# Kernel optimization log

Hardware: AMD Instinct MI355X
Metric: run time of the kernel (lower is better)

## Reference

```python
import jax, jax.numpy as jnp
import numpy as np


def setup_inputs() -> dict:
    key = jax.random.key(0)
    ks = jax.random.split(key, 5)
    B, DEC, ENC, H = 4, 256, 256, 512  # feature_dim = hl_size = 512, mlp hidden = 512
    decoder_states = jax.random.normal(ks[0], (B, DEC, H), dtype=jnp.float32)
    encoder_states = jax.random.normal(ks[1], (B, ENC, H), dtype=jnp.float32)
    ext_mask = jnp.zeros((B, DEC, ENC), dtype=bool)  # self.mask set externally; all-False here
    W_mlp = jax.random.normal(ks[2], (2 * H, H), dtype=jnp.float32) * 0.02  # Linear(2H -> H)
    b_mlp = jnp.zeros((H,), dtype=jnp.float32)
    W_out = jax.random.normal(ks[3], (H, 1), dtype=jnp.float32) * 0.02  # Linear(H -> 1)
    b_out = jnp.zeros((1,), dtype=jnp.float32)
    return {"decoder_states": decoder_states, "encoder_states": encoder_states,
            "ext_mask": ext_mask, "W_mlp": W_mlp, "b_mlp": b_mlp,
            "W_out": W_out, "b_out": b_out}


def reference(decoder_states, encoder_states, ext_mask, W_mlp, b_mlp, W_out, b_out):
    # decoder_states: [B, dec, H]; encoder_states: [B, enc, H]
    H = encoder_states.shape[-1]
    # pad mask: positions where encoder feature-0 equals 0.0 -> [B, 1, enc]
    pad_mask = (encoder_states == 0.0)[:, :, :1]
    pad_mask = jnp.swapaxes(pad_mask, 1, 2)  # [B, 1, enc]
    # cat(enc, dec) @ W_mlp  ==  enc @ W_mlp[:H] + dec @ W_mlp[H:]  (avoids 2H concat)
    enc_proj = jnp.einsum('beh,hm->bem', encoder_states, W_mlp[:H])   # [B, enc, Hm]
    dec_proj = jnp.einsum('bdh,hm->bdm', decoder_states, W_mlp[H:])   # [B, dec, Hm]
    hidden = jnp.tanh(dec_proj[:, :, None, :] + enc_proj[:, None, :, :] + b_mlp)  # [B, dec, enc, Hm]
    attn = jnp.einsum('bdem,mo->bde', hidden, W_out) + b_out[0]       # [B, dec, enc]
    attn = jnp.where(ext_mask, -jnp.inf, attn)
    attn = jnp.where(pad_mask, -jnp.inf, attn)
    attn = jax.nn.softmax(attn, axis=-1)
    context = jnp.einsum('bde,beh->bdh', attn, encoder_states)        # [B, dec, H]
    return (context, attn)
```

## Files before the change

kernel.cpp:

```cpp
#include <hip/hip_runtime.h>
#include <math.h>

#define B 4
#define DEC 256
#define ENC 256
#define HDIM 512

#define TANH_SCALE 2.8853900817779268f
#define LOG2E 1.4426950408889634f

__device__ __forceinline__ float fast_exp2(float x) { return __builtin_amdgcn_exp2f(x); }
__device__ __forceinline__ float fast_rcp(float x)  { return __builtin_amdgcn_rcpf(x); }

typedef __attribute__((ext_vector_type(8))) short bf16x8;
typedef __attribute__((ext_vector_type(4))) short bf16x4;
typedef __attribute__((ext_vector_type(4))) float f32x4;

__device__ __forceinline__ unsigned short bf16_rne(float x) {
    unsigned u = __float_as_uint(x);
    return (unsigned short)((u + 0x7FFFu + ((u >> 16) & 1u)) >> 16);
}
__device__ __forceinline__ float bf16_to_f(unsigned short h) {
    return __uint_as_float((unsigned)h << 16);
}

#define W_OFS(m, k) ((((long)(m) >> 4) << 13) + (((long)(k) >> 3) << 7) + (((m) & 15) << 3) + ((k) & 7))

__global__ __launch_bounds__(256) void convert_kernel(
    const float* __restrict__ enc, const float* __restrict__ dec,
    const float* __restrict__ Wmlp,
    unsigned short* __restrict__ Xh_e, unsigned short* __restrict__ Xl_e,
    unsigned short* __restrict__ Xh_d, unsigned short* __restrict__ Xl_d,
    unsigned short* __restrict__ Wh_e, unsigned short* __restrict__ Wl_e,
    unsigned short* __restrict__ Wh_d, unsigned short* __restrict__ Wl_d)
{
    const int tid = threadIdx.x, z = blockIdx.z;
    if (z < 2) {
        const float* X = z ? dec : enc;
        unsigned short* H = z ? Xh_d : Xh_e;
        unsigned short* L = z ? Xl_d : Xl_e;
        const long i8 = ((long)blockIdx.x * 256 + tid) * 8;
        float4 v0 = *(const float4*)(X + i8);
        float4 v1 = *(const float4*)(X + i8 + 4);
        float xs[8] = {v0.x, v0.y, v0.z, v0.w, v1.x, v1.y, v1.z, v1.w};
        bf16x8 hv, lv;
#pragma unroll
        for (int j = 0; j < 8; ++j) {
            unsigned short h = bf16_rne(xs[j]);
            hv[j] = (short)h;
            lv[j] = (short)bf16_rne(xs[j] - bf16_to_f(h));
        }
        *(bf16x8*)(H + i8) = hv;
        *(bf16x8*)(L + i8) = lv;
    } else {
        const float* Wsrc = Wmlp + (z == 3 ? (long)HDIM * HDIM : 0);
        unsigned short* H = (z == 3) ? Wh_d : Wh_e;
        unsigned short* L = (z == 3) ? Wl_d : Wl_e;
        const int t = blockIdx.x * 256 + tid;
        const int m = t & 511;
        const int k0 = (t >> 9) << 2;
        bf16x4 hv, lv;
#pragma unroll
        for (int j = 0; j < 4; ++j) {
            float x = Wsrc[(long)(k0 + j) * 512 + m];
            unsigned short h = bf16_rne(x);
            hv[j] = (short)h;
            lv[j] = (short)bf16_rne(x - bf16_to_f(h));
        }
        const long ofs = W_OFS(m, k0);
        *(bf16x4*)(H + ofs) = hv;
        *(bf16x4*)(L + ofs) = lv;
    }
}

__global__ __launch_bounds__(256) void proj_mfma_kernel(
    const unsigned short* __restrict__ Xh_e, const unsigned short* __restrict__ Xl_e,
    const unsigned short* __restrict__ Xh_d, const unsigned short* __restrict__ Xl_d,
    const unsigned short* __restrict__ Wh_e, const unsigned short* __restrict__ Wl_e,
    const unsigned short* __restrict__ Wh_d, const unsigned short* __restrict__ Wl_d,
    const float* __restrict__ bmlp,
    float* __restrict__ ET, float* __restrict__ Dmat)
{
    const int tid = threadIdx.x;
    const int wave = tid >> 6, lane = tid & 63;
    const int z = blockIdx.z;
    const int r0w = blockIdx.x * 64 + wave * 16;
    const int m0 = blockIdx.y * 32;
    const unsigned short* Xh = z ? Xh_d : Xh_e;
    const unsigned short* Xl = z ? Xl_d : Xl_e;
    const unsigned short* Wh = z ? Wh_d : Wh_e;
    const unsigned short* Wl = z ? Wl_d : Wl_e;

    const int col = lane & 15;
    const int quad = lane >> 4;

    const unsigned short* pah = Xh + (long)(r0w + col) * 512 + quad * 8;
    const unsigned short* pal = Xl + (long)(r0w + col) * 512 + quad * 8;
    const long bofs = ((long)(m0 >> 4) << 13) + (quad << 7) + (col << 3);
    const unsigned short* pb0h = Wh + bofs;
    const unsigned short* pb0l = Wl + bofs;
    const unsigned short* pb1h = Wh + bofs + 8192;
    const unsigned short* pb1l = Wl + bofs + 8192;

    f32x4 a0h = {0.f,0.f,0.f,0.f}, a0x = {0.f,0.f,0.f,0.f};
    f32x4 a1h = {0.f,0.f,0.f,0.f}, a1x = {0.f,0.f,0.f,0.f};

    bf16x8 Ah = *(const bf16x8*)pah,  Al = *(const bf16x8*)pal;
    bf16x8 B0h = *(const bf16x8*)pb0h, B0l = *(const bf16x8*)pb0l;
    bf16x8 B1h = *(const bf16x8*)pb1h, B1l = *(const bf16x8*)pb1l;

#pragma unroll 1
    for (int k0 = 0; k0 < 512; k0 += 32) {
        bf16x8 nAh = Ah, nAl = Al, nB0h = B0h, nB0l = B0l, nB1h = B1h, nB1l = B1l;
        if (k0 + 32 < 512) {
            nAh = *(const bf16x8*)(pah + k0 + 32);
            nAl = *(const bf16x8*)(pal + k0 + 32);
            const long ko = (long)(k0 + 32) << 4;
            nB0h = *(const bf16x8*)(pb0h + ko);
            nB0l = *(const bf16x8*)(pb0l + ko);
            nB1h = *(const bf16x8*)(pb1h + ko);
            nB1l = *(const bf16x8*)(pb1l + ko);
        }
        a0h = __builtin_amdgcn_mfma_f32_16x16x32_bf16(Ah, B0h, a0h, 0, 0, 0);
        a1h = __builtin_amdgcn_mfma_f32_16x16x32_bf16(Ah, B1h, a1h, 0, 0, 0);
        a0x = __builtin_amdgcn_mfma_f32_16x16x32_bf16(Ah, B0l, a0x, 0, 0, 0);
        a1x = __builtin_amdgcn_mfma_f32_16x16x32_bf16(Ah, B1l, a1x, 0, 0, 0);
        a0x = __builtin_amdgcn_mfma_f32_16x16x32_bf16(Al, B0h, a0x, 0, 0, 0);
        a1x = __builtin_amdgcn_mfma_f32_16x16x32_bf16(Al, B1h, a1x, 0, 0, 0);
        Ah = nAh; Al = nAl; B0h = nB0h; B0l = nB0l; B1h = nB1h; B1l = nB1l;
    }

    if (z == 0) {
        const int batch = r0w >> 8;
        const int e0 = (r0w & 255) + quad * 4;
        float* base = ET + (long)batch * HDIM * ENC;
        float4 v;
        v.x = fast_exp2((a0h[0] + a0x[0]) * TANH_SCALE);
        v.y = fast_exp2((a0h[1] + a0x[1]) * TANH_SCALE);
        v.z = fast_exp2((a0h[2] + a0x[2]) * TANH_SCALE);
        v.w = fast_exp2((a0h[3] + a0x[3]) * TANH_SCALE);
        *(float4*)&base[(long)(m0 + col) * ENC + e0] = v;
        v.x = fast_exp2((a1h[0] + a1x[0]) * TANH_SCALE);
        v.y = fast_exp2((a1h[1] + a1x[1]) * TANH_SCALE);
        v.z = fast_exp2((a1h[2] + a1x[2]) * TANH_SCALE);
        v.w = fast_exp2((a1h[3] + a1x[3]) * TANH_SCALE);
        *(float4*)&base[(long)(m0 + 16 + col) * ENC + e0] = v;
    } else {
        const float bq0 = bmlp[m0 + col];
        const float bq1 = bmlp[m0 + 16 + col];
        const int r = r0w + quad * 4;
#pragma unroll
        for (int i = 0; i < 4; ++i) {
            Dmat[(long)(r + i) * HDIM + m0 + col] =
                fast_exp2((a0h[i] + a0x[i] + bq0) * TANH_SCALE);
            Dmat[(long)(r + i) * HDIM + m0 + 16 + col] =
                fast_exp2((a1h[i] + a1x[i] + bq1) * TANH_SCALE);
        }
    }
}

__global__ __launch_bounds__(256) void attn_partial_kernel(
    const float* __restrict__ Dmat, const float* __restrict__ ET,
    const float* __restrict__ wo, float* __restrict__ part)
{
    __shared__ __align__(16) float ds[4][128];
    __shared__ __align__(16) float wos[128];

    const int tid = threadIdx.x;
    const int b = blockIdx.z, d0 = blockIdx.x * 4, mq = blockIdx.y;
    const int m0q = mq * 128;

    const float* Drow = Dmat + ((long)b * DEC + d0) * HDIM + m0q;
    if (tid < 128) {
#pragma unroll
        for (int r = 0; r < 4; ++r)
            ds[r][tid] = Drow[(long)r * HDIM + tid];
        wos[tid] = wo[m0q + tid];
    }

    const float* ecol = ET + (long)b * HDIM * ENC + (long)m0q * ENC + tid;

    float ev[16], nv[16];
#pragma unroll
    for (int j = 0; j < 16; ++j) ev[j] = ecol[j * ENC];
    __syncthreads();

    float acc[4] = {0.f, 0.f, 0.f, 0.f};
    for (int m = 0; m < 128; m += 16) {
        if (m + 16 < 128) {
#pragma unroll
            for (int j = 0; j < 16; ++j) nv[j] = ecol[(m + 16 + j) * ENC];
        }
        float4 dv[4][4], wv[4];
#pragma unroll
        for (int q = 0; q < 4; ++q) {
#pragma unroll
            for (int r = 0; r < 4; ++r)
                dv[r][q] = *(const float4*)&ds[r][m + q * 4];
            wv[q] = *(const float4*)&wos[m + q * 4];
        }
#pragma unroll
        for (int j = 0; j < 16; ++j) {
            float w = ((const float*)&wv[j >> 2])[j & 3];
#pragma unroll
            for (int r = 0; r < 4; ++r) {
                float t = fmaf(ev[j], ((const float*)&dv[r][j >> 2])[j & 3], 1.0f);
                acc[r] = fmaf(w, fast_rcp(t), acc[r]);
            }
        }
#pragma unroll
        for (int j = 0; j < 16; ++j) ev[j] = nv[j];
    }

    float* pq = part + (long)mq * (B * DEC * ENC);
#pragma unroll
    for (int r = 0; r < 4; ++r)
        pq[((long)b * DEC + d0 + r) * ENC + tid] = acc[r];
}

__global__ __launch_bounds__(256) void attn_finish_kernel(
    const float* __restrict__ part,
    const float* __restrict__ enc, const unsigned char* __restrict__ extm,
    float* __restrict__ attn_out)
{
    __shared__ float red[2][4][2];
    const int tid = threadIdx.x, lane = tid & 63, wave = tid >> 6;
    const int b = blockIdx.y, d0 = blockIdx.x * 2;
    const long g0 = (long)b * DEC + d0;
    const long NQ = (long)B * DEC * ENC;

    float a0 = 0.f, a1 = 0.f;
#pragma unroll
    for (int q = 0; q < 4; ++q) {
        a0 += part[q * NQ + g0 * ENC + tid];
        a1 += part[q * NQ + (g0 + 1) * ENC + tid];
    }

    const int e = tid;
    const bool pad = (enc[((long)b * ENC + e) * HDIM] == 0.0f);
    const bool x0m = extm[g0 * ENC + e] != 0;
    const bool x1m = extm[(g0 + 1) * ENC + e] != 0;
    float l0 = (pad || x0m) ? -__builtin_inff() : -2.0f * a0;
    float l1 = (pad || x1m) ? -__builtin_inff() : -2.0f * a1;

    float m0 = l0, m1 = l1;
#pragma unroll
    for (int off = 32; off >= 1; off >>= 1) {
        m0 = fmaxf(m0, __shfl_xor(m0, off, 64));
        m1 = fmaxf(m1, __shfl_xor(m1, off, 64));
    }
    if (lane == 0) { red[0][wave][0] = m0; red[0][wave][1] = m1; }
    __syncthreads();
    const float gm0 = fmaxf(fmaxf(red[0][0][0], red[0][1][0]), fmaxf(red[0][2][0], red[0][3][0]));
    const float gm1 = fmaxf(fmaxf(red[0][0][1], red[0][1][1]), fmaxf(red[0][2][1], red[0][3][1]));
    float p0 = fast_exp2((l0 - gm0) * LOG2E);
    float p1 = fast_exp2((l1 - gm1) * LOG2E);
    float s0 = p0, s1 = p1;
#pragma unroll
    for (int off = 32; off >= 1; off >>= 1) {
        s0 += __shfl_xor(s0, off, 64);
        s1 += __shfl_xor(s1, off, 64);
    }
    if (lane == 0) { red[1][wave][0] = s0; red[1][wave][1] = s1; }
    __syncthreads();
    const float gs0 = red[1][0][0] + red[1][1][0] + red[1][2][0] + red[1][3][0];
    const float gs1 = red[1][0][1] + red[1][1][1] + red[1][2][1] + red[1][3][1];
    attn_out[g0 * ENC + e] = p0 * fast_rcp(gs0);
    attn_out[(g0 + 1) * ENC + e] = p1 * fast_rcp(gs1);
}

#define C5_LOADW(WB, KOFF)                                                  \
    _Pragma("unroll")                                                       \
    for (int kk = 0; kk < 8; ++kk)                                          \
        WB[kk] = *(const float4*)&We[(long)((KOFF) + kk) * HDIM];

#define C5_FMA(WB, KOFF)                                                    \
    _Pragma("unroll")                                                       \
    for (int q = 0; q < 2; ++q) {                                           \
        float4 xq0 = *(const float4*)&as8[r0l][(KOFF) + q * 4];             \
        float4 xq1 = *(const float4*)&as8[r0l + 1][(KOFF) + q * 4];         \
        _Pragma("unroll")                                                   \
        for (int kk = 0; kk < 4; ++kk) {                                    \
            float4 w = WB[q * 4 + kk];                                      \
            float xv0 = ((const float*)&xq0)[kk];                           \
            float xv1 = ((const float*)&xq1)[kk];                           \
            acc[0][0] = fmaf(xv0, w.x, acc[0][0]);                          \
            acc[0][1] = fmaf(xv0, w.y, acc[0][1]);                          \
            acc[0][2] = fmaf(xv0, w.z, acc[0][2]);                          \
            acc[0][3] = fmaf(xv0, w.w, acc[0][3]);                          \
            acc[1][0] = fmaf(xv1, w.x, acc[1][0]);                          \
            acc[1][1] = fmaf(xv1, w.y, acc[1][1]);                          \
            acc[1][2] = fmaf(xv1, w.z, acc[1][2]);                          \
            acc[1][3] = fmaf(xv1, w.w, acc[1][3]);                          \
        }                                                                   \
    }

__global__ __launch_bounds__(256) void context_kernel(
    const float* __restrict__ attn, const float* __restrict__ enc,
    float* __restrict__ ctx)
{
    __shared__ __align__(16) float as8[8][ENC];
    const int tid = threadIdx.x;
    const int tx = tid & 63, ty = tid >> 6;
    const int r0 = blockIdx.x * 8;
    const int b = r0 >> 8;
    const int h0 = blockIdx.y * 256 + tx * 4;
    const int r0l = ty * 2;
    const float* We = enc + (long)b * ENC * HDIM + h0;

    {
        const float* ag = attn + (long)r0 * ENC;
#pragma unroll
        for (int i = 0; i < 2; ++i) {
            int idx = (tid + i * 256) * 4;
            *(float4*)&as8[0][idx] = *(const float4*)&ag[idx];
        }
    }

    float acc[2][4] = {};
    float4 Wa[8], Wb[8];
    C5_LOADW(Wa, 0)
    __syncthreads();

    for (int k0 = 0; k0 < ENC; k0 += 16) {
        C5_LOADW(Wb, k0 + 8)
        C5_FMA(Wa, k0)
        if (k0 + 16 < ENC) { C5_LOADW(Wa, k0 + 16) }
        C5_FMA(Wb, k0 + 8)
    }

#pragma unroll
    for (int i = 0; i < 2; ++i)
        *(float4*)&ctx[(long)(r0 + r0l + i) * HDIM + h0] =
            make_float4(acc[i][0], acc[i][1], acc[i][2], acc[i][3]);
}

extern "C" void kernel_launch(void* const* d_in, const int* in_sizes, int n_in,
                              void* d_out, int out_size, void* d_ws, size_t ws_size,
                              hipStream_t stream) {
    const float* dec = (const float*)d_in[0];
    const float* enc = (const float*)d_in[1];
    const unsigned char* extm = (const unsigned char*)d_in[2];
    const float* Wmlp = (const float*)d_in[3];
    const float* bmlp = (const float*)d_in[4];
    const float* Wout = (const float*)d_in[5];

    float* ctx = (float*)d_out;
    float* attn = ctx + (size_t)B * DEC * HDIM;

    const size_t F = (size_t)B * DEC * HDIM;
    float* ET = (float*)d_ws;
    float* Dmat = ET + F;
    unsigned short* Xh_e = (unsigned short*)(Dmat + F);
    unsigned short* Xl_e = Xh_e + F;
    unsigned short* Xh_d = Xl_e + F;
    unsigned short* Xl_d = Xh_d + F;
    unsigned short* Wh_e = Xl_d + F;
    unsigned short* Wl_e = Wh_e + HDIM * HDIM;
    unsigned short* Wh_d = Wl_e + HDIM * HDIM;
    unsigned short* Wl_d = Wh_d + HDIM * HDIM;
    float* part = (float*)(Wl_d + HDIM * HDIM);

    convert_kernel<<<dim3(256, 1, 4), 256, 0, stream>>>(
        enc, dec, Wmlp, Xh_e, Xl_e, Xh_d, Xl_d, Wh_e, Wl_e, Wh_d, Wl_d);
    proj_mfma_kernel<<<dim3(16, 16, 2), 256, 0, stream>>>(
        Xh_e, Xl_e, Xh_d, Xl_d, Wh_e, Wl_e, Wh_d, Wl_d, bmlp, ET, Dmat);
    attn_partial_kernel<<<dim3(DEC / 4, 4, B), 256, 0, stream>>>(Dmat, ET, Wout, part);
    attn_finish_kernel<<<dim3(DEC / 2, B), 256, 0, stream>>>(part, enc, extm, attn);
    context_kernel<<<dim3(128, 2), 256, 0, stream>>>(attn, enc, ctx);
}
```

Before: 118.9 us.

## Fuse attention partials, softmax and context into one kernel

```diff
diff --git a/kernel.cpp b/kernel.cpp
--- a/kernel.cpp
+++ b/kernel.cpp
@@ -159,26 +159,29 @@
     }
 }
 
-__global__ __launch_bounds__(256) void attn_partial_kernel(
+__global__ __launch_bounds__(512) void attn_ctx_kernel(
     const float* __restrict__ Dmat, const float* __restrict__ ET,
-    const float* __restrict__ wo, float* __restrict__ part)
+    const float* __restrict__ wo,
+    const float* __restrict__ enc, const unsigned char* __restrict__ extm,
+    float* __restrict__ attn_out, float* __restrict__ ctx)
 {
-    __shared__ __align__(16) float ds[4][128];
-    __shared__ __align__(16) float wos[128];
+    __shared__ __align__(16) float ds[4][HDIM];
+    __shared__ __align__(16) float wos[HDIM];
+    __shared__ __align__(16) float p2[2][4][ENC];
+    __shared__ __align__(16) float as4[4][ENC];
+    __shared__ float redm[4][4];
+    __shared__ float reds[4][4];
 
     const int tid = threadIdx.x;
-    const int b = blockIdx.z, d0 = blockIdx.x * 4, mq = blockIdx.y;
-    const int m0q = mq * 128;
-
-    const float* Drow = Dmat + ((long)b * DEC + d0) * HDIM + m0q;
-    if (tid < 128) {
-#pragma unroll
-        for (int r = 0; r < 4; ++r)
-            ds[r][tid] = Drow[(long)r * HDIM + tid];
-        wos[tid] = wo[m0q + tid];
-    }
-
-    const float* ecol = ET + (long)b * HDIM * ENC + (long)m0q * ENC + tid;
+    const int b = blockIdx.z, d0 = blockIdx.x * 4;
+    const long g0 = (long)b * DEC + d0;
+
+    ((float4*)ds)[tid] = ((const float4*)(Dmat + g0 * HDIM))[tid];
+    if (tid < 128) ((float4*)wos)[tid] = ((const float4*)wo)[tid];
+
+    const int ty = tid >> 8;
+    const int e = tid & 255;
+    const float* ecol = ET + (long)b * HDIM * ENC + (long)(ty * 256) * ENC + e;
 
     float ev[16], nv[16];
 #pragma unroll
@@ -186,18 +189,19 @@
     __syncthreads();
 
     float acc[4] = {0.f, 0.f, 0.f, 0.f};
-    for (int m = 0; m < 128; m += 16) {
-        if (m + 16 < 128) {
+    for (int m = 0; m < 256; m += 16) {
+        if (m + 16 < 256) {
 #pragma unroll
             for (int j = 0; j < 16; ++j) nv[j] = ecol[(m + 16 + j) * ENC];
         }
+        const int mb = ty * 256 + m;
         float4 dv[4][4], wv[4];
 #pragma unroll
         for (int q = 0; q < 4; ++q) {
 #pragma unroll
             for (int r = 0; r < 4; ++r)
-                dv[r][q] = *(const float4*)&ds[r][m + q * 4];
-            wv[q] = *(const float4*)&wos[m + q * 4];
+                dv[r][q] = *(const float4*)&ds[r][mb + q * 4];
+            wv[q] = *(const float4*)&wos[mb + q * 4];
         }
 #pragma unroll
         for (int j = 0; j < 16; ++j) {
@@ -212,127 +216,99 @@
         for (int j = 0; j < 16; ++j) ev[j] = nv[j];
     }
 
-    float* pq = part + (long)mq * (B * DEC * ENC);
-#pragma unroll
-    for (int r = 0; r < 4; ++r)
-        pq[((long)b * DEC + d0 + r) * ENC + tid] = acc[r];
-}
-
-__global__ __launch_bounds__(256) void attn_finish_kernel(
-    const float* __restrict__ part,
-    const float* __restrict__ enc, const unsigned char* __restrict__ extm,
-    float* __restrict__ attn_out)
-{
-    __shared__ float red[2][4][2];
-    const int tid = threadIdx.x, lane = tid & 63, wave = tid >> 6;
-    const int b = blockIdx.y, d0 = blockIdx.x * 2;
-    const long g0 = (long)b * DEC + d0;
-    const long NQ = (long)B * DEC * ENC;
-
-    float a0 = 0.f, a1 = 0.f;
-#pragma unroll
-    for (int q = 0; q < 4; ++q) {
-        a0 += part[q * NQ + g0 * ENC + tid];
-        a1 += part[q * NQ + (g0 + 1) * ENC + tid];
-    }
-
-    const int e = tid;
-    const bool pad = (enc[((long)b * ENC + e) * HDIM] == 0.0f);
-    const bool x0m = extm[g0 * ENC + e] != 0;
-    const bool x1m = extm[(g0 + 1) * ENC + e] != 0;
-    float l0 = (pad || x0m) ? -__builtin_inff() : -2.0f * a0;
-    float l1 = (pad || x1m) ? -__builtin_inff() : -2.0f * a1;
-
-    float m0 = l0, m1 = l1;
-#pragma unroll
-    for (int off = 32; off >= 1; off >>= 1) {
-        m0 = fmaxf(m0, __shfl_xor(m0, off, 64));
-        m1 = fmaxf(m1, __shfl_xor(m1, off, 64));
-    }
-    if (lane == 0) { red[0][wave][0] = m0; red[0][wave][1] = m1; }
-    __syncthreads();
-    const float gm0 = fmaxf(fmaxf(red[0][0][0], red[0][1][0]), fmaxf(red[0][2][0], red[0][3][0]));
-    const float gm1 = fmaxf(fmaxf(red[0][0][1], red[0][1][1]), fmaxf(red[0][2][1], red[0][3][1]));
-    float p0 = fast_exp2((l0 - gm0) * LOG2E);
-    float p1 = fast_exp2((l1 - gm1) * LOG2E);
-    float s0 = p0, s1 = p1;
-#pragma unroll
-    for (int off = 32; off >= 1; off >>= 1) {
-        s0 += __shfl_xor(s0, off, 64);
-        s1 += __shfl_xor(s1, off, 64);
-    }
-    if (lane == 0) { red[1][wave][0] = s0; red[1][wave][1] = s1; }
-    __syncthreads();
-    const float gs0 = red[1][0][0] + red[1][1][0] + red[1][2][0] + red[1][3][0];
-    const float gs1 = red[1][0][1] + red[1][1][1] + red[1][2][1] + red[1][3][1];
-    attn_out[g0 * ENC + e] = p0 * fast_rcp(gs0);
-    attn_out[(g0 + 1) * ENC + e] = p1 * fast_rcp(gs1);
-}
-
-#define C5_LOADW(WB, KOFF)                                                  \
-    _Pragma("unroll")                                                       \
-    for (int kk = 0; kk < 8; ++kk)                                          \
-        WB[kk] = *(const float4*)&We[(long)((KOFF) + kk) * HDIM];
-
-#define C5_FMA(WB, KOFF)                                                    \
-    _Pragma("unroll")                                                       \
-    for (int q = 0; q < 2; ++q) {                                           \
-        float4 xq0 = *(const float4*)&as8[r0l][(KOFF) + q * 4];             \
-        float4 xq1 = *(const float4*)&as8[r0l + 1][(KOFF) + q * 4];         \
-        _Pragma("unroll")                                                   \
-        for (int kk = 0; kk < 4; ++kk) {                                    \
-            float4 w = WB[q * 4 + kk];                                      \
-            float xv0 = ((const float*)&xq0)[kk];                           \
-            float xv1 = ((const float*)&xq1)[kk];                           \
-            acc[0][0] = fmaf(xv0, w.x, acc[0][0]);                          \
-            acc[0][1] = fmaf(xv0, w.y, acc[0][1]);                          \
-            acc[0][2] = fmaf(xv0, w.z, acc[0][2]);                          \
-            acc[0][3] = fmaf(xv0, w.w, acc[0][3]);                          \
-            acc[1][0] = fmaf(xv1, w.x, acc[1][0]);                          \
-            acc[1][1] = fmaf(xv1, w.y, acc[1][1]);                          \
-            acc[1][2] = fmaf(xv1, w.z, acc[1][2]);                          \
-            acc[1][3] = fmaf(xv1, w.w, acc[1][3]);                          \
-        }                                                                   \
-    }
-
-__global__ __launch_bounds__(256) void context_kernel(
-    const float* __restrict__ attn, const float* __restrict__ enc,
-    float* __restrict__ ctx)
-{
-    __shared__ __align__(16) float as8[8][ENC];
-    const int tid = threadIdx.x;
-    const int tx = tid & 63, ty = tid >> 6;
-    const int r0 = blockIdx.x * 8;
-    const int b = r0 >> 8;
-    const int h0 = blockIdx.y * 256 + tx * 4;
-    const int r0l = ty * 2;
-    const float* We = enc + (long)b * ENC * HDIM + h0;
-
-    {
-        const float* ag = attn + (long)r0 * ENC;
-#pragma unroll
-        for (int i = 0; i < 2; ++i) {
-            int idx = (tid + i * 256) * 4;
-            *(float4*)&as8[0][idx] = *(const float4*)&ag[idx];
-        }
-    }
-
-    float acc[2][4] = {};
-    float4 Wa[8], Wb[8];
-    C5_LOADW(Wa, 0)
-    __syncthreads();
-
-    for (int k0 = 0; k0 < ENC; k0 += 16) {
-        C5_LOADW(Wb, k0 + 8)
-        C5_FMA(Wa, k0)
-        if (k0 + 16 < ENC) { C5_LOADW(Wa, k0 + 16) }
-        C5_FMA(Wb, k0 + 8)
-    }
-
-#pragma unroll
-    for (int i = 0; i < 2; ++i)
-        *(float4*)&ctx[(long)(r0 + r0l + i) * HDIM + h0] =
-            make_float4(acc[i][0], acc[i][1], acc[i][2], acc[i][3]);
+#pragma unroll
+    for (int r = 0; r < 4; ++r) p2[ty][r][e] = acc[r];
+    __syncthreads();
+
+    float l[4], p[4];
+    const int wave = tid >> 6, lane = tid & 63;
+    if (ty == 0) {
+        const bool pad = (enc[((long)b * ENC + e) * HDIM] == 0.0f);
+#pragma unroll
+        for (int r = 0; r < 4; ++r) {
+            float a = p2[0][r][e] + p2[1][r][e];
+            bool xm = extm[(g0 + r) * ENC + e] != 0;
+            l[r] = (pad || xm) ? -__builtin_inff() : -2.0f * a;
+        }
+        float mx[4] = {l[0], l[1], l[2], l[3]};
+#pragma unroll
+        for (int off = 32; off >= 1; off >>= 1) {
+#pragma unroll
+            for (int r = 0; r < 4; ++r)
+                mx[r] = fmaxf(mx[r], __shfl_xor(mx[r], off, 64));
+        }
+        if (lane == 0) {
+#pragma unroll
+            for (int r = 0; r < 4; ++r) redm[wave][r] = mx[r];
+        }
+    }
+    __syncthreads();
+    if (ty == 0) {
+        float s[4];
+#pragma unroll
+        for (int r = 0; r < 4; ++r) {
+            float gm = fmaxf(fmaxf(redm[0][r], redm[1][r]),
+                             fmaxf(redm[2][r], redm[3][r]));
+            p[r] = fast_exp2((l[r] - gm) * LOG2E);
+            s[r] = p[r];
+        }
+#pragma unroll
+        for (int off = 32; off >= 1; off >>= 1) {
+#pragma unroll
+            for (int r = 0; r < 4; ++r)
+                s[r] += __shfl_xor(s[r], off, 64);
+        }
+        if (lane == 0) {
+#pragma unroll
+            for (int r = 0; r < 4; ++r) reds[wave][r] = s[r];
+        }
+    }
+    __syncthreads();
+    if (ty == 0) {
+#pragma unroll
+        for (int r = 0; r < 4; ++r) {
+            float gs = reds[0][r] + reds[1][r] + reds[2][r] + reds[3][r];
+            float pr = p[r] * fast_rcp(gs);
+            attn_out[(g0 + r) * ENC + e] = pr;
+            as4[r][e] = pr;
+        }
+    }
+    __syncthreads();
+
+    const int r = tid >> 7;
+    const int hh = (tid & 127) * 4;
+    const float* ew = enc + (long)b * ENC * HDIM + hh;
+    float4 acc4 = {0.f, 0.f, 0.f, 0.f};
+    float4 wa[4], wb[4];
+#pragma unroll
+    for (int j = 0; j < 4; ++j) wa[j] = *(const float4*)(ew + (long)j * HDIM);
+    for (int e0 = 0; e0 < ENC; e0 += 8) {
+#pragma unroll
+        for (int j = 0; j < 4; ++j)
+            wb[j] = *(const float4*)(ew + (long)(e0 + 4 + j) * HDIM);
+#pragma unroll
+        for (int j = 0; j < 4; ++j) {
+            float a = as4[r][e0 + j];
+            acc4.x = fmaf(a, wa[j].x, acc4.x);
+            acc4.y = fmaf(a, wa[j].y, acc4.y);
+            acc4.z = fmaf(a, wa[j].z, acc4.z);
+            acc4.w = fmaf(a, wa[j].w, acc4.w);
+        }
+        if (e0 + 8 < ENC) {
+#pragma unroll
+            for (int j = 0; j < 4; ++j)
+                wa[j] = *(const float4*)(ew + (long)(e0 + 8 + j) * HDIM);
+        }
+#pragma unroll
+        for (int j = 0; j < 4; ++j) {
+            float a = as4[r][e0 + 4 + j];
+            acc4.x = fmaf(a, wb[j].x, acc4.x);
+            acc4.y = fmaf(a, wb[j].y, acc4.y);
+            acc4.z = fmaf(a, wb[j].z, acc4.z);
+            acc4.w = fmaf(a, wb[j].w, acc4.w);
+        }
+    }
+    *(float4*)&ctx[(g0 + r) * HDIM + hh] = acc4;
 }
 
 extern "C" void kernel_launch(void* const* d_in, const int* in_sizes, int n_in,
@@ -359,13 +335,11 @@
     unsigned short* Wl_e = Wh_e + HDIM * HDIM;
     unsigned short* Wh_d = Wl_e + HDIM * HDIM;
     unsigned short* Wl_d = Wh_d + HDIM * HDIM;
-    float* part = (float*)(Wl_d + HDIM * HDIM);
 
     convert_kernel<<<dim3(256, 1, 4), 256, 0, stream>>>(
         enc, dec, Wmlp, Xh_e, Xl_e, Xh_d, Xl_d, Wh_e, Wl_e, Wh_d, Wl_d);
     proj_mfma_kernel<<<dim3(16, 16, 2), 256, 0, stream>>>(
         Xh_e, Xl_e, Xh_d, Xl_d, Wh_e, Wl_e, Wh_d, Wl_d, bmlp, ET, Dmat);
-    attn_partial_kernel<<<dim3(DEC / 4, 4, B), 256, 0, stream>>>(Dmat, ET, Wout, part);
-    attn_finish_kernel<<<dim3(DEC / 2, B), 256, 0, stream>>>(part, enc, extm, attn);
-    context_kernel<<<dim3(128, 2), 256, 0, stream>>>(attn, enc, ctx);
-}
+    attn_ctx_kernel<<<dim3(DEC / 4, 1, B), 512, 0, stream>>>(
+        Dmat, ET, Wout, enc, extm, attn, ctx);
+}
```

New measurement: 121.3 us. +2.0%, slower.
